# Performance work log

Hardware: AMD Instinct MI355X
Metric: run time of the kernel (lower is better)

## Reference

```python
import jax, jax.numpy as jnp
import numpy as np

THR = 1.0   # snntorch default threshold
BETA = 0.9  # beta_val from init_kwargs (clamped to [0,1] in snntorch)
ALPHA_SG = 2.0  # snntorch ATan surrogate default alpha

T, B, IN, H1, H2, OUT = 50, 256, 1536, 4096, 4096, 64


@jax.custom_vjp
def spike_fn(mem_shift):
    # Heaviside spike with ATan surrogate gradient (snntorch default)
    return (mem_shift > 0).astype(mem_shift.dtype)

def _spike_fwd(m):
    return spike_fn(m), m

def _spike_bwd(m, g):
    grad = (ALPHA_SG / 2.0) / (1.0 + (jnp.pi / 2.0 * ALPHA_SG * m) ** 2)
    return (g * grad,)

spike_fn.defvjp(_spike_fwd, _spike_bwd)


def setup_inputs() -> dict:
    key = jax.random.key(0)
    ks = jax.random.split(key, 7)
    spike_seq = (jax.random.uniform(ks[0], (T, B, IN)) < 0.3).astype(jnp.float32)
    def lin(k, fan_out, fan_in):
        bound = 1.0 / np.sqrt(fan_in)
        kw, kb = jax.random.split(k)
        W = jax.random.uniform(kw, (fan_out, fan_in), minval=-bound, maxval=bound, dtype=jnp.float32)
        b = jax.random.uniform(kb, (fan_out,), minval=-bound, maxval=bound, dtype=jnp.float32)
        return W, b
    W1, b1 = lin(ks[1], H1, IN)
    W2, b2 = lin(ks[2], H2, H1)
    W3, b3 = lin(ks[3], OUT, H2)
    return {"spike_seq": spike_seq, "W1": W1, "b1": b1, "W2": W2, "b2": b2, "W3": W3, "b3": b3}


def _lif_step(mem, cur):
    # snntorch Leaky, reset_mechanism='subtract': reset is computed from the
    # PREVIOUS membrane and detached; then mem = beta*mem + cur - reset*thr.
    reset = jax.lax.stop_gradient((mem > THR).astype(cur.dtype))
    mem = BETA * mem + cur - reset * THR
    spk = spike_fn(mem - THR)
    return spk, mem


def reference(spike_seq, W1, b1, W2, b2, W3, b3):
    batch = spike_seq.shape[1]
    dt = spike_seq.dtype
    m1 = jnp.zeros((batch, W1.shape[0]), dt)
    m2 = jnp.zeros((batch, W2.shape[0]), dt)
    m3 = jnp.zeros((batch, W3.shape[0]), dt)
    acc = jnp.zeros((batch, W3.shape[0]), dt)

    def step(carry, x_t):
        m1, m2, m3, acc = carry
        s1, m1 = _lif_step(m1, x_t @ W1.T + b1)
        s2, m2 = _lif_step(m2, s1 @ W2.T + b2)
        s3, m3 = _lif_step(m3, s2 @ W3.T + b3)
        return (m1, m2, m3, acc + s3), None

    (m1, m2, m3, acc), _ = jax.lax.scan(step, (m1, m2, m3, acc), spike_seq)
    return acc
```

## Files before the change

kernel.cpp:

```cpp
#include <hip/hip_runtime.h>
#include <stdint.h>
#include <stddef.h>
#include <math.h>


#define T_STEPS 50
#define BATCH   256
#define N_H     4096
#define DEN     8355711

typedef unsigned short u16;
typedef __attribute__((ext_vector_type(4))) int i32x4;
typedef __attribute__((ext_vector_type(4))) float f32x4;

#define GLL16(gp, lp) __builtin_amdgcn_global_load_lds( \
    (const __attribute__((address_space(1))) void*)(gp), \
    (__attribute__((address_space(3))) void*)(lp), 16, 0, 0)

__global__ __launch_bounds__(256) void zero_ws(float4* __restrict__ p) {
    p[(size_t)blockIdx.x * 256 + threadIdx.x] = make_float4(0.f, 0.f, 0.f, 0.f);
}

__device__ inline void digits3(float w, float inv_s, int& h, int& m, int& l) {
    int V = (int)rintf(w * inv_s);
    V = min(max(V, -DEN), DEN);
    l = ((V + 128) & 255) - 128;
    const int V2 = (V - l) >> 8;
    m = ((V2 + 128) & 255) - 128;
    h = (V2 - m) >> 8;
}

__global__ __launch_bounds__(256)
void split3_i8(const float4* __restrict__ W, char* __restrict__ P,
               size_t plane_elems, float inv_s)
{
    const size_t i = (size_t)blockIdx.x * 256 + threadIdx.x;
    const float4 w = W[i];
    int h0,m0,l0,h1,m1,l1,h2,m2,l2,h3,m3,l3;
    digits3(w.x, inv_s, h0, m0, l0);
    digits3(w.y, inv_s, h1, m1, l1);
    digits3(w.z, inv_s, h2, m2, l2);
    digits3(w.w, inv_s, h3, m3, l3);
    const uint32_t ph = (uint32_t)(uint8_t)h0 | ((uint32_t)(uint8_t)h1 << 8) |
                        ((uint32_t)(uint8_t)h2 << 16) | ((uint32_t)(uint8_t)h3 << 24);
    const uint32_t pm = (uint32_t)(uint8_t)m0 | ((uint32_t)(uint8_t)m1 << 8) |
                        ((uint32_t)(uint8_t)m2 << 16) | ((uint32_t)(uint8_t)m3 << 24);
    const uint32_t pl = (uint32_t)(uint8_t)l0 | ((uint32_t)(uint8_t)l1 << 8) |
                        ((uint32_t)(uint8_t)l2 << 16) | ((uint32_t)(uint8_t)l3 << 24);
    *(uint32_t*)&P[4 * i]                   = ph;
    *(uint32_t*)&P[plane_elems + 4 * i]     = pm;
    *(uint32_t*)&P[2 * plane_elems + 4 * i] = pl;
}

__global__ __launch_bounds__(256)
void xcvt_i8(const float4* __restrict__ in, uint32_t* __restrict__ out) {
    const size_t i = (size_t)blockIdx.x * 256 + threadIdx.x;
    const float4 v = in[i];
    out[i] = (uint32_t)(v.x > 0.5f) | ((uint32_t)(v.y > 0.5f) << 8) |
             ((uint32_t)(v.z > 0.5f) << 16) | ((uint32_t)(v.w > 0.5f) << 24);
}

template<int K>
__global__ __launch_bounds__(512, 2)
void gemm_planes_ring(const char* __restrict__ A, const char* __restrict__ Wp,
                      float* __restrict__ cur, float s_base)
{
    const int ITERS = 3 * K / 64;
    const int SLOT  = 24576;
    extern __shared__ char Lds[];

    const int tid  = threadIdx.x;
    const int wave = tid >> 6, lane = tid & 63;
    const int wr = wave >> 1, wc = wave & 1;

    const int bid   = blockIdx.x;
    const int cbase = (((bid & 7) << 2) + ((bid >> 3) & 3)) * 128;
    const int abase = (bid >> 5) * 256;

    i32x4 acc[4][4];
    f32x4 facc[4][4];
#pragma unroll
    for (int i = 0; i < 4; ++i)
#pragma unroll
        for (int j = 0; j < 4; ++j) { acc[i][j] = (i32x4)(0); facc[i][j] = (f32x4)(0.f); }

    const int soff = tid * 16;
    const int rs   = soff >> 6;
    const int cs   = (soff >> 4) & 3;
    const int kbs  = ((cs ^ ((rs >> 1) & 3)) << 4);
    const size_t aoff0 = (size_t)(abase + rs) * K + kbs;
    const size_t aoff1 = aoff0 + (size_t)128 * K;
    const size_t boff  = (size_t)(cbase + rs) * K + kbs;
    const int dstA0 = wave * 1024;
    const int dstA1 = 8192 + wave * 1024;
    const int dstB  = 16384 + wave * 1024;

    const int rlo = lane & 15, rhi = lane >> 4;
    const int qr  = (rlo >> 1) & 3;
    const int rdA = (wr * 64 + rlo) * 64 + ((rhi ^ qr) << 4);
    const int rdB = 16384 + (wc * 64 + rlo) * 64 + ((rhi ^ qr) << 4);

    auto stage = [&](int u) {
        const int pn = (u * 64) / K;
        const int kn = u * 64 - pn * K;
        char* slot = Lds + (u & 3) * SLOT;
        const char* ak = A + kn;
        const char* bk = Wp + (size_t)pn * ((size_t)N_H * K) + kn;
        GLL16(ak + aoff0, slot + dstA0);
        GLL16(ak + aoff1, slot + dstA1);
        GLL16(bk + boff,  slot + dstB);
    };

    stage(0); stage(1); stage(2);
    asm volatile("s_waitcnt vmcnt(6)" ::: "memory");
    __builtin_amdgcn_s_barrier();
    asm volatile("" ::: "memory");

    i32x4 avA[4], bvA[4], avB[4], bvB[4];
    {
        const char* nb = Lds;
#pragma unroll
        for (int i = 0; i < 4; ++i) avA[i] = *(const i32x4*)(nb + rdA + i * 1024);
#pragma unroll
        for (int j = 0; j < 4; ++j) bvA[j] = *(const i32x4*)(nb + rdB + j * 1024);
    }

#define RING_BODY(tt, avC, bvC, avN, bvN)                                     \
    {                                                                         \
        if ((tt) + 2 < ITERS) { asm volatile("s_waitcnt vmcnt(3)" ::: "memory"); } \
        else                  { asm volatile("s_waitcnt vmcnt(0)" ::: "memory"); } \
        __builtin_amdgcn_s_barrier();                                         \
        asm volatile("" ::: "memory");                                        \
        if ((tt) + 3 < ITERS) stage((tt) + 3);                                \
        if ((tt) + 1 < ITERS) {                                               \
            const char* nb_ = Lds + (((tt) + 1) & 3) * SLOT;                  \
            _Pragma("unroll")                                                 \
            for (int i = 0; i < 4; ++i)                                       \
                avN[i] = *(const i32x4*)(nb_ + rdA + i * 1024);               \
            _Pragma("unroll")                                                 \
            for (int j = 0; j < 4; ++j)                                       \
                bvN[j] = *(const i32x4*)(nb_ + rdB + j * 1024);               \
        }                                                                     \
        __builtin_amdgcn_s_setprio(1);                                        \
        _Pragma("unroll")                                                     \
        for (int i = 0; i < 4; ++i)                                           \
            _Pragma("unroll")                                                 \
            for (int j = 0; j < 4; ++j)                                       \
                acc[i][j] = __builtin_amdgcn_mfma_i32_16x16x64_i8(            \
                    avC[i], bvC[j], acc[i][j], 0, 0, 0);                      \
        __builtin_amdgcn_s_setprio(0);                                        \
        if (((((tt) + 1) * 64) % K) == 0) {                                   \
            const int p_ = ((tt) * 64) / K;                                   \
            const float sc_ = s_base * (float)(65536 >> (8 * p_));            \
            _Pragma("unroll")                                                 \
            for (int i = 0; i < 4; ++i)                                       \
                _Pragma("unroll")                                             \
                for (int j = 0; j < 4; ++j) {                                 \
                    _Pragma("unroll")                                         \
                    for (int r = 0; r < 4; ++r)                               \
                        facc[i][j][r] += sc_ * (float)acc[i][j][r];           \
                    acc[i][j] = (i32x4)(0);                                   \
                }                                                             \
        }                                                                     \
    }

    for (int t = 0; t < ITERS; t += 2) {
        RING_BODY(t,     avA, bvA, avB, bvB);
        RING_BODY(t + 1, avB, bvB, avA, bvA);
    }
#undef RING_BODY

    const int orow = abase + wr * 64 + rhi * 4;
    const int ocol = cbase + wc * 64 + rlo;
#pragma unroll
    for (int i = 0; i < 4; ++i)
#pragma unroll
        for (int j = 0; j < 4; ++j)
#pragma unroll
            for (int r = 0; r < 4; ++r)
                cur[(size_t)(orow + i * 16 + r) * N_H + ocol + j * 16] = facc[i][j][r];
}

template<int K>
__global__ __launch_bounds__(256, 2)
void gemm_planes(const char* __restrict__ A, const char* __restrict__ Wp,
                 float* __restrict__ cur, float s_base)
{
    const int ITERS = 3 * K / 64;
    __shared__ char As[2 * 8192];
    __shared__ char Bs[2 * 8192];

    const int tid  = threadIdx.x;
    const int wave = tid >> 6, lane = tid & 63;
    const int wm = wave >> 1, wn = wave & 1;

    const int bid   = blockIdx.x;
    const int cbase = (((bid & 7) << 2) + ((bid >> 3) & 3)) * 128;
    const int abase = (bid >> 5) * 128;

    i32x4 acc[4][4];
    f32x4 facc[4][4];
#pragma unroll
    for (int i = 0; i < 4; ++i)
#pragma unroll
        for (int j = 0; j < 4; ++j) { acc[i][j] = (i32x4)(0); facc[i][j] = (f32x4)(0.f); }

    const int soff0 = wave * 2048 + lane * 16;
    const int soff1 = soff0 + 1024;
    const int r0 = soff0 >> 6, r1 = soff1 >> 6;
    const int kb0 = ((((soff0 >> 4) & 3) ^ ((r0 >> 1) & 3)) << 4);
    const int kb1 = ((((soff1 >> 4) & 3) ^ ((r1 >> 1) & 3)) << 4);

    const size_t aoff0 = (size_t)(abase + r0) * K + kb0;
    const size_t aoff1 = (size_t)(abase + r1) * K + kb1;
    const size_t boff0 = (size_t)(cbase + r0) * K + kb0;
    const size_t boff1 = (size_t)(cbase + r1) * K + kb1;

    const int sbase = wave * 2048;

    const int rlo = lane & 15, rhi = lane >> 4;
    const int qr = (rlo >> 1) & 3;
    const int rdA = (wm * 64 + rlo) * 64 + ((rhi ^ qr) << 4);
    const int rdB = (wn * 64 + rlo) * 64 + ((rhi ^ qr) << 4);

    {
        GLL16(A + aoff0, As + sbase);
        GLL16(A + aoff1, As + sbase + 1024);
        GLL16(Wp + boff0, Bs + sbase);
        GLL16(Wp + boff1, Bs + sbase + 1024);
    }
    __syncthreads();

    for (int it = 0; it < ITERS; ++it) {
        const int buf = (it & 1) * 8192;
        if (it + 1 < ITERS) {
            const int fn = (it + 1) * 64;
            const int pn = fn / K;
            const int kn = fn - pn * K;
            const int nbuf = 8192 - buf;
            const char* ak = A + kn;
            const char* bk = Wp + (size_t)pn * ((size_t)N_H * K) + kn;
            GLL16(ak + aoff0, As + nbuf + sbase);
            GLL16(ak + aoff1, As + nbuf + sbase + 1024);
            GLL16(bk + boff0, Bs + nbuf + sbase);
            GLL16(bk + boff1, Bs + nbuf + sbase + 1024);
        }

        const char* pAf = As + buf + rdA;
        const char* pBf = Bs + buf + rdB;
        i32x4 av[4], bv[4];
#pragma unroll
        for (int i = 0; i < 4; ++i) av[i] = *(const i32x4*)(pAf + i * 1024);
#pragma unroll
        for (int j = 0; j < 4; ++j) bv[j] = *(const i32x4*)(pBf + j * 1024);
#pragma unroll
        for (int i = 0; i < 4; ++i)
#pragma unroll
            for (int j = 0; j < 4; ++j)
                acc[i][j] = __builtin_amdgcn_mfma_i32_16x16x64_i8(
                    av[i], bv[j], acc[i][j], 0, 0, 0);

        if ((((it + 1) * 64) % K) == 0) {
            const int p = (it * 64) / K;
            const float sc = s_base * (float)(65536 >> (8 * p));
#pragma unroll
            for (int i = 0; i < 4; ++i)
#pragma unroll
                for (int j = 0; j < 4; ++j) {
#pragma unroll
                    for (int r = 0; r < 4; ++r)
                        facc[i][j][r] += sc * (float)acc[i][j][r];
                    acc[i][j] = (i32x4)(0);
                }
        }
        __syncthreads();
    }

    const int orow = abase + wm * 64 + rhi * 4;
    const int ocol = cbase + wn * 64 + rlo;
#pragma unroll
    for (int i = 0; i < 4; ++i)
#pragma unroll
        for (int j = 0; j < 4; ++j)
#pragma unroll
            for (int r = 0; r < 4; ++r)
                cur[(size_t)(orow + i * 16 + r) * N_H + ocol + j * 16] = facc[i][j][r];
}

__global__ __launch_bounds__(256, 2)
void gemm3_i8(const char* __restrict__ A, const char* __restrict__ W3p,
              float* __restrict__ part3, float s_base)
{
    __shared__ char As[2 * 8192];
    __shared__ char Bs[2 * 4096];

    const int tid  = threadIdx.x;
    const int wave = tid >> 6, lane = tid & 63;
    const int wm = wave >> 1, wn = wave & 1;

    const int rowbase = blockIdx.x * 128;
    const int z = blockIdx.y;
    const int p = z >> 1;
    const int kstart = (z & 1) * 2048;

    i32x4 acc[4][2];
#pragma unroll
    for (int i = 0; i < 4; ++i)
#pragma unroll
        for (int j = 0; j < 2; ++j) acc[i][j] = (i32x4)(0);

    const int soff0 = wave * 2048 + lane * 16;
    const int soff1 = soff0 + 1024;
    const int r0 = soff0 >> 6, r1 = soff1 >> 6;
    const int kb0 = ((((soff0 >> 4) & 3) ^ ((r0 >> 1) & 3)) << 4);
    const int kb1 = ((((soff1 >> 4) & 3) ^ ((r1 >> 1) & 3)) << 4);
    const int soffB = tid * 16;
    const int rB = soffB >> 6;
    const int kbB = ((((soffB >> 4) & 3) ^ ((rB >> 1) & 3)) << 4);

    const size_t aoff0 = (size_t)(rowbase + r0) * 4096 + kb0;
    const size_t aoff1 = (size_t)(rowbase + r1) * 4096 + kb1;
    const size_t boff  = (size_t)rB * 4096 + kbB;

    const char* Bp = W3p + (size_t)p * 64 * 4096;
    const int sbase = wave * 2048;
    const int sbaseB = wave * 1024;

    const int rlo = lane & 15, rhi = lane >> 4;
    const int qr = (rlo >> 1) & 3;
    const int rdA = (wm * 64 + rlo) * 64 + ((rhi ^ qr) << 4);
    const int rdB = (wn * 32 + rlo) * 64 + ((rhi ^ qr) << 4);

    {
        GLL16(A + kstart + aoff0, As + sbase);
        GLL16(A + kstart + aoff1, As + sbase + 1024);
        GLL16(Bp + kstart + boff, Bs + sbaseB);
    }
    __syncthreads();

    for (int it = 0; it < 32; ++it) {
        const int bufA = (it & 1) * 8192;
        const int bufB = (it & 1) * 4096;
        if (it + 1 < 32) {
            const int kn = kstart + (it + 1) * 64;
            GLL16(A + kn + aoff0, As + (8192 - bufA) + sbase);
            GLL16(A + kn + aoff1, As + (8192 - bufA) + sbase + 1024);
            GLL16(Bp + kn + boff, Bs + (4096 - bufB) + sbaseB);
        }

        const char* pAf = As + bufA + rdA;
        const char* pBf = Bs + bufB + rdB;
        i32x4 av[4], bv[2];
#pragma unroll
        for (int i = 0; i < 4; ++i) av[i] = *(const i32x4*)(pAf + i * 1024);
#pragma unroll
        for (int j = 0; j < 2; ++j) bv[j] = *(const i32x4*)(pBf + j * 1024);
#pragma unroll
        for (int i = 0; i < 4; ++i)
#pragma unroll
            for (int j = 0; j < 2; ++j)
                acc[i][j] = __builtin_amdgcn_mfma_i32_16x16x64_i8(
                    av[i], bv[j], acc[i][j], 0, 0, 0);
        __syncthreads();
    }

    const float sc = s_base * (float)(65536 >> (8 * p));
    float* pout = part3 + (size_t)z * (12800 * 64);
    const int orow = rowbase + wm * 64 + rhi * 4;
    const int ocol = wn * 32 + rlo;
#pragma unroll
    for (int i = 0; i < 4; ++i)
#pragma unroll
        for (int j = 0; j < 2; ++j)
#pragma unroll
            for (int r = 0; r < 4; ++r)
                pout[(size_t)(orow + i * 16 + r) * 64 + ocol + j * 16] =
                    (float)acc[i][j][r] * sc;
}

__global__ __launch_bounds__(256)
void lif_scan(const float* __restrict__ cur, const float* __restrict__ bias,
              float* __restrict__ mem, char* __restrict__ sout)
{
    const int i4  = blockIdx.x * 256 + threadIdx.x;
    const int col = (i4 << 2) & (N_H - 1);
    const int b   = i4 >> 10;
    const float4 bv = *(const float4*)&bias[col];
    const size_t mbase = (size_t)b * N_H + col;
    float4 m = *(const float4*)&mem[mbase];

    for (int t = 0; t < 25; ++t) {
        const size_t off = ((size_t)t * BATCH + b) * N_H + col;
        const float4 cv = *(const float4*)&cur[off];
        float4 mn;
        { const float c = cv.x + bv.x;
          mn.x = 0.9f * m.x + c - ((m.x > 1.0f) ? 1.0f : 0.0f); }
        { const float c = cv.y + bv.y;
          mn.y = 0.9f * m.y + c - ((m.y > 1.0f) ? 1.0f : 0.0f); }
        { const float c = cv.z + bv.z;
          mn.z = 0.9f * m.z + c - ((m.z > 1.0f) ? 1.0f : 0.0f); }
        { const float c = cv.w + bv.w;
          mn.w = 0.9f * m.w + c - ((m.w > 1.0f) ? 1.0f : 0.0f); }
        const uint32_t sp = (uint32_t)(mn.x > 1.0f) | ((uint32_t)(mn.y > 1.0f) << 8) |
                            ((uint32_t)(mn.z > 1.0f) << 16) | ((uint32_t)(mn.w > 1.0f) << 24);
        *(uint32_t*)&sout[off] = sp;
        m = mn;
    }
    *(float4*)&mem[mbase] = m;
}

template<int NG>
__global__ __launch_bounds__(256)
void lif3_scan(const float* __restrict__ part, const float* __restrict__ b3,
               float* __restrict__ out)
{
    const int g = blockIdx.x * 256 + threadIdx.x;
    const int j = g & 63;
    const int b = g >> 6;
    const float bj = b3[j];
    float m = 0.f, accum = 0.f;
    for (int t = 0; t < T_STEPS; ++t) {
        const size_t row = (size_t)t * 256 + b;
        float cur = bj;
#pragma unroll
        for (int q = 0; q < NG; ++q)
            cur += part[(size_t)q * (12800 * 64) + row * 64 + j];
        const float reset = (m > 1.0f) ? 1.0f : 0.0f;
        m = 0.9f * m + cur - reset;
        accum += (m > 1.0f) ? 1.0f : 0.0f;
    }
    out[g] = accum;
}

template<int K, bool PACK_BITS>
__global__ __launch_bounds__(512)
void gemm_lif(const float* __restrict__ A, const float* __restrict__ W,
              const float* __restrict__ bias, float* __restrict__ mem,
              float* __restrict__ s_f32, uint32_t* __restrict__ s_bits)
{
    __shared__ float Asf[32][68];
    __shared__ float Wsf[32][68];
    __shared__ uint8_t us[64][64];

    const int tid = threadIdx.x;
    const int abase = blockIdx.y * 64;
    const int cbase = blockIdx.x * 64;
    const int tx = tid & 15;
    const int ty = tid >> 4;

    float acc[2][4];
#pragma unroll
    for (int i = 0; i < 2; ++i)
#pragma unroll
        for (int j = 0; j < 4; ++j) acc[i][j] = 0.f;

    const int lrow = tid >> 3;
    const int lg = tid & 7;

    for (int k0 = 0; k0 < K; k0 += 32) {
        const float4 av = *(const float4*)&A[(size_t)(abase + lrow) * K + k0 + lg * 4];
        const float4 wv = *(const float4*)&W[(size_t)(cbase + lrow) * K + k0 + lg * 4];
        __syncthreads();
        Asf[lg * 4 + 0][lrow] = av.x; Asf[lg * 4 + 1][lrow] = av.y;
        Asf[lg * 4 + 2][lrow] = av.z; Asf[lg * 4 + 3][lrow] = av.w;
        Wsf[lg * 4 + 0][lrow] = wv.x; Wsf[lg * 4 + 1][lrow] = wv.y;
        Wsf[lg * 4 + 2][lrow] = wv.z; Wsf[lg * 4 + 3][lrow] = wv.w;
        __syncthreads();
#pragma unroll
        for (int kk = 0; kk < 32; ++kk) {
            const float2 a2 = *(const float2*)&Asf[kk][ty * 2];
            const float4 b4 = *(const float4*)&Wsf[kk][tx * 4];
            acc[0][0] += a2.x * b4.x; acc[0][1] += a2.x * b4.y;
            acc[0][2] += a2.x * b4.z; acc[0][3] += a2.x * b4.w;
            acc[1][0] += a2.y * b4.x; acc[1][1] += a2.y * b4.y;
            acc[1][2] += a2.y * b4.z; acc[1][3] += a2.y * b4.w;
        }
    }

    const int r0 = abase + ty * 2;
    const int c0loc = tx * 4;
    const int c0 = cbase + c0loc;
    const float4 bv = *(const float4*)&bias[c0];

#pragma unroll
    for (int i = 0; i < 2; ++i) {
        const size_t off = (size_t)(r0 + i) * N_H + c0;
        const float4 mp = *(const float4*)&mem[off];
        float4 mn, sp;
        { float cur = acc[i][0] + bv.x;
          mn.x = 0.9f * mp.x + cur - ((mp.x > 1.0f) ? 1.0f : 0.0f);
          sp.x = (mn.x > 1.0f) ? 1.0f : 0.0f; }
        { float cur = acc[i][1] + bv.y;
          mn.y = 0.9f * mp.y + cur - ((mp.y > 1.0f) ? 1.0f : 0.0f);
          sp.y = (mn.y > 1.0f) ? 1.0f : 0.0f; }
        { float cur = acc[i][2] + bv.z;
          mn.z = 0.9f * mp.z + cur - ((mp.z > 1.0f) ? 1.0f : 0.0f);
          sp.z = (mn.z > 1.0f) ? 1.0f : 0.0f; }
        { float cur = acc[i][3] + bv.w;
          mn.w = 0.9f * mp.w + cur - ((mp.w > 1.0f) ? 1.0f : 0.0f);
          sp.w = (mn.w > 1.0f) ? 1.0f : 0.0f; }
        *(float4*)&mem[off] = mn;
        if constexpr (!PACK_BITS) {
            *(float4*)&s_f32[off] = sp;
        } else {
            us[ty * 2 + i][c0loc + 0] = (uint8_t)sp.x;
            us[ty * 2 + i][c0loc + 1] = (uint8_t)sp.y;
            us[ty * 2 + i][c0loc + 2] = (uint8_t)sp.z;
            us[ty * 2 + i][c0loc + 3] = (uint8_t)sp.w;
        }
    }

    if constexpr (PACK_BITS) {
        __syncthreads();
        if (tid < 128) {
            const int r = tid >> 1;
            const int w = tid & 1;
            uint32_t bits = 0;
#pragma unroll
            for (int b = 0; b < 32; ++b)
                bits |= ((uint32_t)us[r][w * 32 + b]) << b;
            s_bits[(size_t)(abase + r) * 128 + (cbase >> 5) + w] = bits;
        }
    }
}

__global__ __launch_bounds__(256)
void gemm3_bits(const uint32_t* __restrict__ s_bits, const float* __restrict__ W3,
                float* __restrict__ part)
{
    __shared__ float Asf[32][68];
    __shared__ float Wsf[32][68];

    const int tid = threadIdx.x;
    const int rowbase = blockIdx.x * 64;
    const int ks = blockIdx.y;
    const int tx = tid & 15;
    const int ty = tid >> 4;

    float acc[4][4];
#pragma unroll
    for (int i = 0; i < 4; ++i)
#pragma unroll
        for (int j = 0; j < 4; ++j) acc[i][j] = 0.f;

    const int r  = tid & 63;
    const int q  = tid >> 6;
    const int wr = tid >> 3;
    const int wg = tid & 7;

    for (int c = 0; c < 32; ++c) {
        const int k0 = ks * 1024 + c * 32;
        const uint32_t word = s_bits[(size_t)(rowbase + r) * 128 + (k0 >> 5)];
        const float4 wv0 = *(const float4*)&W3[(size_t)wr * 4096 + k0 + wg * 4];
        const float4 wv1 = *(const float4*)&W3[(size_t)(wr + 32) * 4096 + k0 + wg * 4];
        __syncthreads();
#pragma unroll
        for (int u = 0; u < 8; ++u)
            Asf[q * 8 + u][r] = (float)((word >> (q * 8 + u)) & 1u);
        Wsf[wg * 4 + 0][wr] = wv0.x;
        Wsf[wg * 4 + 1][wr] = wv0.y;
        Wsf[wg * 4 + 2][wr] = wv0.z;
        Wsf[wg * 4 + 3][wr] = wv0.w;
        Wsf[wg * 4 + 0][wr + 32] = wv1.x;
        Wsf[wg * 4 + 1][wr + 32] = wv1.y;
        Wsf[wg * 4 + 2][wr + 32] = wv1.z;
        Wsf[wg * 4 + 3][wr + 32] = wv1.w;
        __syncthreads();
#pragma unroll
        for (int kk = 0; kk < 32; ++kk) {
            const float4 a4 = *(const float4*)&Asf[kk][ty * 4];
            const float4 b4 = *(const float4*)&Wsf[kk][tx * 4];
            acc[0][0] += a4.x * b4.x; acc[0][1] += a4.x * b4.y;
            acc[0][2] += a4.x * b4.z; acc[0][3] += a4.x * b4.w;
            acc[1][0] += a4.y * b4.x; acc[1][1] += a4.y * b4.y;
            acc[1][2] += a4.y * b4.z; acc[1][3] += a4.y * b4.w;
            acc[2][0] += a4.z * b4.x; acc[2][1] += a4.z * b4.y;
            acc[2][2] += a4.z * b4.z; acc[2][3] += a4.z * b4.w;
            acc[3][0] += a4.w * b4.x; acc[3][1] += a4.w * b4.y;
            acc[3][2] += a4.w * b4.z; acc[3][3] += a4.w * b4.w;
        }
    }
#pragma unroll
    for (int i = 0; i < 4; ++i) {
        float4 v = make_float4(acc[i][0], acc[i][1], acc[i][2], acc[i][3]);
        *(float4*)&part[((size_t)ks * 12800 + rowbase + ty * 4 + i) * 64 + tx * 4] = v;
    }
}

extern "C" void kernel_launch(void* const* d_in, const int* in_sizes, int n_in,
                              void* d_out, int out_size, void* d_ws, size_t ws_size,
                              hipStream_t stream)
{
    const float* x  = (const float*)d_in[0];
    const float* W1 = (const float*)d_in[1];
    const float* b1 = (const float*)d_in[2];
    const float* W2 = (const float*)d_in[3];
    const float* b2 = (const float*)d_in[4];
    const float* W3 = (const float*)d_in[5];
    const float* b3 = (const float*)d_in[6];

    char* ws = (char*)d_ws;

    const size_t oW1p = 0;
    const size_t oW2p = 18874368;
    const size_t oW3p = 69206016;
    const size_t oXi8 = 69992448;
    const size_t oS1  = 89653248;
    const size_t oS2  = 115867648;
    const size_t oM1  = 168296448;
    const size_t oM2  = 172490752;
    const size_t oCur = 176685056;
    const size_t NEED = 281542656;

    const double bnd1 = 1.0 / sqrt(1536.0);
    const double bnd2 = 1.0 / 64.0;
    const double bnd3 = 1.0 / 64.0;
    const float inv1 = (float)((double)DEN / bnd1), sb1 = (float)(bnd1 / (double)DEN);
    const float inv2 = (float)((double)DEN / bnd2), sb2 = (float)(bnd2 / (double)DEN);
    const float inv3 = (float)((double)DEN / bnd3), sb3 = (float)(bnd3 / (double)DEN);

    static const bool ring_ok = []() {
        hipError_t e1 = hipFuncSetAttribute(
            reinterpret_cast<const void*>(&gemm_planes_ring<1536>),
            hipFuncAttributeMaxDynamicSharedMemorySize, 98304);
        hipError_t e2 = hipFuncSetAttribute(
            reinterpret_cast<const void*>(&gemm_planes_ring<4096>),
            hipFuncAttributeMaxDynamicSharedMemorySize, 98304);
        return e1 == hipSuccess && e2 == hipSuccess;
    }();

    if (ws_size >= NEED) {
        char*  W1p  = ws + oW1p;
        char*  W2p  = ws + oW2p;
        char*  W3p  = ws + oW3p;
        char*  xi8  = ws + oXi8;
        char*  s1   = ws + oS1;
        char*  s2   = ws + oS2;
        float* m1   = (float*)(ws + oM1);
        float* m2   = (float*)(ws + oM2);
        float* cur  = (float*)(ws + oCur);
        float* part3 = cur;

        split3_i8<<<6144, 256, 0, stream>>>((const float4*)W1, W1p,
                                            (size_t)4096 * 1536, inv1);
        split3_i8<<<16384, 256, 0, stream>>>((const float4*)W2, W2p,
                                             (size_t)4096 * 4096, inv2);
        split3_i8<<<256, 256, 0, stream>>>((const float4*)W3, W3p,
                                           (size_t)64 * 4096, inv3);
        xcvt_i8<<<19200, 256, 0, stream>>>((const float4*)x, (uint32_t*)xi8);
        zero_ws<<<2048, 256, 0, stream>>>((float4*)m1);

        const size_t chunk_rows = (size_t)25 * BATCH;
        for (int chunk = 0; chunk < 2; ++chunk) {
            if (ring_ok) {
                gemm_planes_ring<1536><<<800, 512, 98304, stream>>>(
                    xi8 + chunk * chunk_rows * 1536, W1p, cur, sb1);
            } else {
                gemm_planes<1536><<<1600, 256, 0, stream>>>(
                    xi8 + chunk * chunk_rows * 1536, W1p, cur, sb1);
            }
            lif_scan<<<1024, 256, 0, stream>>>(cur, b1, m1, s1);
            if (ring_ok) {
                gemm_planes_ring<4096><<<800, 512, 98304, stream>>>(
                    s1, W2p, cur, sb2);
            } else {
                gemm_planes<4096><<<1600, 256, 0, stream>>>(s1, W2p, cur, sb2);
            }
            lif_scan<<<1024, 256, 0, stream>>>(cur, b2, m2,
                                               s2 + chunk * chunk_rows * N_H);
        }
        gemm3_i8<<<dim3(100, 6), 256, 0, stream>>>(s2, W3p, part3, sb3);
        lif3_scan<6><<<64, 256, 0, stream>>>(part3, b3, (float*)d_out);
    } else {
        float*    m1     = (float*)(ws);
        float*    m2     = (float*)(ws + (size_t)4 * 1024 * 1024);
        float*    s1f    = (float*)(ws + (size_t)8 * 1024 * 1024);
        uint32_t* s2bits = (uint32_t*)(ws + (size_t)12 * 1024 * 1024);
        float*    part   = (float*)(ws + (size_t)20 * 1024 * 1024);

        zero_ws<<<2048, 256, 0, stream>>>((float4*)m1);
        for (int t = 0; t < T_STEPS; ++t) {
            gemm_lif<1536, false><<<dim3(64, 4), 512, 0, stream>>>(
                x + (size_t)t * BATCH * 1536, W1, b1, m1, s1f, nullptr);
            gemm_lif<4096, true><<<dim3(64, 4), 512, 0, stream>>>(
                s1f, W2, b2, m2, nullptr, s2bits + (size_t)t * BATCH * 128);
        }
        gemm3_bits<<<dim3(200, 4), 256, 0, stream>>>(s2bits, W3, part);
        lif3_scan<4><<<64, 256, 0, stream>>>(part, b3, (float*)d_out);
    }
}
```

Before: 1.389 ms.

## Restructure int8 plane GEMM main loop into phased 4-slot pipeline with explicit barriers

Replaces the double-buffered register ring loop with a phase scheme. Each phase loads one LDS slot's fragments into a single register set, issues the next global-to-LDS stage, then runs the MFMAs behind a barrier and a sched_barrier, with a final barrier at the end of each phase. The loop is unrolled by four so that slot indices and vmcnt waits are compile-time constants. Launch bounds drop from two blocks per CU to one, which frees registers but may lower occupancy, and the extra barriers per iteration add synchronisation cost.

```diff
diff --git a/kernel.cpp b/kernel.cpp
--- a/kernel.cpp
+++ b/kernel.cpp
@@ -61,9 +61,9 @@
 }
 
 template<int K>
-__global__ __launch_bounds__(512, 2)
-void gemm_planes_ring(const char* __restrict__ A, const char* __restrict__ Wp,
-                      float* __restrict__ cur, float s_base)
+__global__ __launch_bounds__(512, 1)
+void gemm_planes_ph(const char* __restrict__ A, const char* __restrict__ Wp,
+                    float* __restrict__ cur, float s_base)
 {
     const int ITERS = 3 * K / 64;
     const int SLOT  = 24576;
@@ -100,10 +100,10 @@
     const int rdA = (wr * 64 + rlo) * 64 + ((rhi ^ qr) << 4);
     const int rdB = 16384 + (wc * 64 + rlo) * 64 + ((rhi ^ qr) << 4);
 
-    auto stage = [&](int u) {
+    auto stage = [&](int u, int slot_off) {
         const int pn = (u * 64) / K;
         const int kn = u * 64 - pn * K;
-        char* slot = Lds + (u & 3) * SLOT;
+        char* slot = Lds + slot_off;
         const char* ak = A + kn;
         const char* bk = Wp + (size_t)pn * ((size_t)N_H * K) + kn;
         GLL16(ak + aoff0, slot + dstA0);
@@ -111,64 +111,69 @@
         GLL16(bk + boff,  slot + dstB);
     };
 
-    stage(0); stage(1); stage(2);
-    asm volatile("s_waitcnt vmcnt(6)" ::: "memory");
-    __builtin_amdgcn_s_barrier();
-    asm volatile("" ::: "memory");
-
-    i32x4 avA[4], bvA[4], avB[4], bvB[4];
-    {
-        const char* nb = Lds;
-#pragma unroll
-        for (int i = 0; i < 4; ++i) avA[i] = *(const i32x4*)(nb + rdA + i * 1024);
-#pragma unroll
-        for (int j = 0; j < 4; ++j) bvA[j] = *(const i32x4*)(nb + rdB + j * 1024);
-    }
-
-#define RING_BODY(tt, avC, bvC, avN, bvN)                                     \
+    i32x4 av[4], bv[4];
+
+#define FOLD(tt)                                                              \
+    if (((((tt) + 1) * 64) % K) == 0) {                                       \
+        const int p_ = ((tt) * 64) / K;                                       \
+        const float sc_ = s_base * (float)(65536 >> (8 * p_));                \
+        _Pragma("unroll")                                                     \
+        for (int i = 0; i < 4; ++i)                                           \
+            _Pragma("unroll")                                                 \
+            for (int j = 0; j < 4; ++j) {                                     \
+                _Pragma("unroll")                                             \
+                for (int r = 0; r < 4; ++r)                                   \
+                    facc[i][j][r] += sc_ * (float)acc[i][j][r];               \
+                acc[i][j] = (i32x4)(0);                                       \
+            }                                                                 \
+    }
+
+#define PH(tt, SN, SS, NW, GS, DOW)                                           \
     {                                                                         \
-        if ((tt) + 2 < ITERS) { asm volatile("s_waitcnt vmcnt(3)" ::: "memory"); } \
-        else                  { asm volatile("s_waitcnt vmcnt(0)" ::: "memory"); } \
-        __builtin_amdgcn_s_barrier();                                         \
-        asm volatile("" ::: "memory");                                        \
-        if ((tt) + 3 < ITERS) stage((tt) + 3);                                \
-        if ((tt) + 1 < ITERS) {                                               \
-            const char* nb_ = Lds + (((tt) + 1) & 3) * SLOT;                  \
+        {                                                                     \
+            const char* nb_ = Lds + (SN) * SLOT;                              \
             _Pragma("unroll")                                                 \
             for (int i = 0; i < 4; ++i)                                       \
-                avN[i] = *(const i32x4*)(nb_ + rdA + i * 1024);               \
+                av[i] = *(const i32x4*)(nb_ + rdA + i * 1024);                \
             _Pragma("unroll")                                                 \
             for (int j = 0; j < 4; ++j)                                       \
-                bvN[j] = *(const i32x4*)(nb_ + rdB + j * 1024);               \
+                bv[j] = *(const i32x4*)(nb_ + rdB + j * 1024);                \
         }                                                                     \
+        if (GS) stage((tt) + 3, (SS) * SLOT);                                 \
+        __builtin_amdgcn_s_barrier();                                         \
+        __builtin_amdgcn_sched_barrier(0);                                    \
         __builtin_amdgcn_s_setprio(1);                                        \
         _Pragma("unroll")                                                     \
         for (int i = 0; i < 4; ++i)                                           \
             _Pragma("unroll")                                                 \
             for (int j = 0; j < 4; ++j)                                       \
                 acc[i][j] = __builtin_amdgcn_mfma_i32_16x16x64_i8(            \
-                    avC[i], bvC[j], acc[i][j], 0, 0, 0);                      \
+                    av[i], bv[j], acc[i][j], 0, 0, 0);                        \
         __builtin_amdgcn_s_setprio(0);                                        \
-        if (((((tt) + 1) * 64) % K) == 0) {                                   \
-            const int p_ = ((tt) * 64) / K;                                   \
-            const float sc_ = s_base * (float)(65536 >> (8 * p_));            \
-            _Pragma("unroll")                                                 \
-            for (int i = 0; i < 4; ++i)                                       \
-                _Pragma("unroll")                                             \
-                for (int j = 0; j < 4; ++j) {                                 \
-                    _Pragma("unroll")                                         \
-                    for (int r = 0; r < 4; ++r)                               \
-                        facc[i][j][r] += sc_ * (float)acc[i][j][r];           \
-                    acc[i][j] = (i32x4)(0);                                   \
-                }                                                             \
-        }                                                                     \
-    }
-
-    for (int t = 0; t < ITERS; t += 2) {
-        RING_BODY(t,     avA, bvA, avB, bvB);
-        RING_BODY(t + 1, avB, bvB, avA, bvA);
-    }
-#undef RING_BODY
+        if (DOW) { asm volatile("s_waitcnt vmcnt(" #NW ")" ::: "memory"); }   \
+        FOLD(tt);                                                             \
+        __builtin_amdgcn_s_barrier();                                         \
+    }
+
+    stage(0, 0); stage(1, SLOT); stage(2, 2 * SLOT);
+    asm volatile("s_waitcnt vmcnt(6)" ::: "memory");
+    __builtin_amdgcn_s_barrier();
+    asm volatile("" ::: "memory");
+
+    int t = 0;
+    for (; t + 7 < ITERS; t += 4) {
+        PH(t + 0, 0, 3, 6, 1, 1);
+        PH(t + 1, 1, 0, 6, 1, 1);
+        PH(t + 2, 2, 1, 6, 1, 1);
+        PH(t + 3, 3, 2, 6, 1, 1);
+    }
+    PH(t + 0, 0, 3, 6, 1, 1);
+    PH(t + 1, 1, 0, 3, 0, 1);
+    PH(t + 2, 2, 1, 0, 0, 1);
+    PH(t + 3, 3, 2, 0, 0, 0);
+
+#undef PH
+#undef FOLD
 
     const int orow = abase + wr * 64 + rhi * 4;
     const int ocol = cbase + wc * 64 + rlo;
@@ -619,12 +624,12 @@
     const float inv2 = (float)((double)DEN / bnd2), sb2 = (float)(bnd2 / (double)DEN);
     const float inv3 = (float)((double)DEN / bnd3), sb3 = (float)(bnd3 / (double)DEN);
 
-    static const bool ring_ok = []() {
+    static const bool ph_ok = []() {
         hipError_t e1 = hipFuncSetAttribute(
-            reinterpret_cast<const void*>(&gemm_planes_ring<1536>),
+            reinterpret_cast<const void*>(&gemm_planes_ph<1536>),
             hipFuncAttributeMaxDynamicSharedMemorySize, 98304);
         hipError_t e2 = hipFuncSetAttribute(
-            reinterpret_cast<const void*>(&gemm_planes_ring<4096>),
+            reinterpret_cast<const void*>(&gemm_planes_ph<4096>),
             hipFuncAttributeMaxDynamicSharedMemorySize, 98304);
         return e1 == hipSuccess && e2 == hipSuccess;
     }();
@@ -652,16 +657,16 @@
 
         const size_t chunk_rows = (size_t)25 * BATCH;
         for (int chunk = 0; chunk < 2; ++chunk) {
-            if (ring_ok) {
-                gemm_planes_ring<1536><<<800, 512, 98304, stream>>>(
+            if (ph_ok) {
+                gemm_planes_ph<1536><<<800, 512, 98304, stream>>>(
                     xi8 + chunk * chunk_rows * 1536, W1p, cur, sb1);
             } else {
                 gemm_planes<1536><<<1600, 256, 0, stream>>>(
                     xi8 + chunk * chunk_rows * 1536, W1p, cur, sb1);
             }
             lif_scan<<<1024, 256, 0, stream>>>(cur, b1, m1, s1);
-            if (ring_ok) {
-                gemm_planes_ring<4096><<<800, 512, 98304, stream>>>(
+            if (ph_ok) {
+                gemm_planes_ph<4096><<<800, 512, 98304, stream>>>(
                     s1, W2p, cur, sb2);
             } else {
                 gemm_planes<4096><<<1600, 256, 0, stream>>>(s1, W2p, cur, sb2);
```

After: 1.302 ms. -6.3%, faster.
